# Kernel optimization log

Hardware: AMD Instinct MI355X
Metric: run time of the kernel (lower is better)

## Reference

```python
import jax, jax.numpy as jnp
import numpy as np

GROUPS = 32
EPS = 1e-5


def group_norm(x, w, b):
    # x: [B, C, H, W]
    B, C, H, W = x.shape
    g = x.reshape(B, GROUPS, C // GROUPS, H * W)
    mu = g.mean(axis=(2, 3), keepdims=True)
    var = g.var(axis=(2, 3), keepdims=True)
    g = (g - mu) * jax.lax.rsqrt(var + EPS)
    g = g.reshape(B, C, H, W)
    return g * w[None, :, None, None] + b[None, :, None, None]


def setup_inputs() -> dict:
    key = jax.random.key(0)
    ks = jax.random.split(key, 6)
    B, C, H, W = 4, 512, 64, 64
    s = 1.0 / np.sqrt(C)  # sane init scale for 1x1 conv weights
    return {
        "x": jax.random.normal(ks[0], (B, C, H, W), dtype=jnp.float32),
        "gn_w": jnp.ones((C,), dtype=jnp.float32),
        "gn_b": jnp.zeros((C,), dtype=jnp.float32),
        "wq": jax.random.normal(ks[1], (C, C), dtype=jnp.float32) * s,
        "bq": jnp.zeros((C,), dtype=jnp.float32),
        "wk": jax.random.normal(ks[2], (C, C), dtype=jnp.float32) * s,
        "bk": jnp.zeros((C,), dtype=jnp.float32),
        "wv": jax.random.normal(ks[3], (C, C), dtype=jnp.float32) * s,
        "bv": jnp.zeros((C,), dtype=jnp.float32),
        "wp": jax.random.normal(ks[4], (C, C), dtype=jnp.float32) * s,
        "bp": jnp.zeros((C,), dtype=jnp.float32),
    }


def reference(x, gn_w, gn_b, wq, bq, wk, bk, wv, bv, wp, bp):
    B, C, H, W = x.shape
    h = group_norm(x, gn_w, gn_b)
    # tokens: [B, N, C], N = H*W
    t = h.reshape(B, C, H * W).transpose(0, 2, 1)
    # 1x1 convs == per-token linear: y_d = sum_c w[d,c] * t_c + b_d
    q = jnp.einsum('bnc,dc->bnd', t, wq) + bq
    k = jnp.einsum('bnc,dc->bnd', t, wk) + bk
    v = jnp.einsum('bnc,dc->bnd', t, wv) + bv
    scale = 1.0 / jnp.sqrt(jnp.asarray(C, dtype=x.dtype))
    qk = jnp.einsum('bnd,bmd->bnm', q, k) * scale  # [B, N, N]
    attn = jax.nn.softmax(qk, axis=-1)
    out = jnp.einsum('bnm,bmd->bnd', attn, v)  # [B, N, C]
    proj = jnp.einsum('bnc,dc->bnd', out, wp) + bp
    return x + proj.transpose(0, 2, 1).reshape(B, C, H, W)
```

## Files before the change

kernel.cpp:

```cpp
#include <hip/hip_runtime.h>
#include <stdint.h>

#define B_   4
#define C_   512
#define N_   4096
#define G_   32
#define CPG  16
#define EPS  1e-5f

typedef __attribute__((ext_vector_type(8))) short bf16x8;
typedef __attribute__((ext_vector_type(4))) float f32x4;
typedef __attribute__((ext_vector_type(4))) int   i32x4;

__device__ __forceinline__ unsigned short f2bf(float f){
  union { float f; uint32_t u; } v; v.f = f;
  uint32_t r = v.u + 0x7fffu + ((v.u >> 16) & 1u);
  return (unsigned short)(r >> 16);
}
__device__ __forceinline__ float bf2f(unsigned short h){
  union { uint32_t u; float f; } v; v.u = ((uint32_t)h) << 16;
  return v.f;
}

__device__ __forceinline__ void gload16(const unsigned short* g, unsigned short* l){
  __builtin_amdgcn_global_load_lds(
      (__attribute__((address_space(1))) void*)(g),
      (__attribute__((address_space(3))) void*)(l), 16, 0, 0);
}
__device__ __forceinline__ void gload16i(const signed char* g, signed char* l){
  __builtin_amdgcn_global_load_lds(
      (__attribute__((address_space(1))) void*)(g),
      (__attribute__((address_space(3))) void*)(l), 16, 0, 0);
}

__global__ __launch_bounds__(256) void cvt_kernel(const float* __restrict__ in,
                                                  unsigned short* __restrict__ out, int n){
  int i = (blockIdx.x * 256 + threadIdx.x) * 4;
  if (i < n){
    float4 v = *(const float4*)(in + i);
    out[i+0] = f2bf(v.x); out[i+1] = f2bf(v.y);
    out[i+2] = f2bf(v.z); out[i+3] = f2bf(v.w);
  }
}

__global__ __launch_bounds__(256) void concat_bias_k(const float* __restrict__ bq,
                                                     const float* __restrict__ bk,
                                                     const float* __restrict__ bv,
                                                     float* __restrict__ b){
  int i = blockIdx.x * 256 + threadIdx.x;
  if (i < 1536)
    b[i] = (i < 512) ? bq[i] : ((i < 1024) ? bk[i-512] : bv[i-1024]);
}

__global__ __launch_bounds__(256) void gn_stats_k(const float* __restrict__ x,
                                                  float* __restrict__ stats){
  int bg = blockIdx.x;
  const float* p = x + (size_t)bg * (CPG * N_);
  float s = 0.f, ss = 0.f;
  for (int i = threadIdx.x * 4; i < CPG * N_; i += 256 * 4){
    float4 v = *(const float4*)(p + i);
    s  += v.x + v.y + v.z + v.w;
    ss += v.x*v.x + v.y*v.y + v.z*v.z + v.w*v.w;
  }
  #pragma unroll
  for (int o = 32; o >= 1; o >>= 1){ s += __shfl_xor(s, o); ss += __shfl_xor(ss, o); }
  __shared__ float sb[8];
  int w = threadIdx.x >> 6;
  if ((threadIdx.x & 63) == 0){ sb[w] = s; sb[4+w] = ss; }
  __syncthreads();
  if (threadIdx.x == 0){
    float S  = sb[0]+sb[1]+sb[2]+sb[3];
    float SS = sb[4]+sb[5]+sb[6]+sb[7];
    const float inv = 1.f / (CPG * N_);
    float mu  = S * inv;
    float var = SS * inv - mu * mu;
    stats[bg*2]   = mu;
    stats[bg*2+1] = rsqrtf(var + EPS);
  }
}

__global__ __launch_bounds__(256) void gn_apply_k(const float* __restrict__ x,
                                                  const float* __restrict__ stats,
                                                  const float* __restrict__ gw,
                                                  const float* __restrict__ gb,
                                                  unsigned short* __restrict__ t){
  int b  = blockIdx.z;
  int c0 = blockIdx.y * 64, n0 = blockIdx.x * 64;
  __shared__ float tile[64][65];
  for (int i = threadIdx.x; i < 64*64; i += 256){
    int cl = i >> 6, nl = i & 63;
    int c = c0 + cl;
    int g = c >> 4;
    float mu = stats[(b*G_+g)*2], rs = stats[(b*G_+g)*2+1];
    float v = x[((size_t)b*C_ + c)*N_ + n0 + nl];
    tile[cl][nl] = (v - mu) * rs * gw[c] + gb[c];
  }
  __syncthreads();
  for (int i = threadIdx.x; i < 64*64; i += 256){
    int nl = i >> 6, cl = i & 63;
    t[((size_t)b*N_ + n0 + nl)*C_ + c0 + cl] = f2bf(tile[cl][nl]);
  }
}

__global__ __launch_bounds__(256) void quant_qk_k(const unsigned short* __restrict__ qkv,
                                                  signed char* __restrict__ q8,
                                                  signed char* __restrict__ k8,
                                                  float invs){
  size_t idx = (size_t)blockIdx.x * 256 + threadIdx.x;
  size_t tok = idx >> 6;
  int ch = (int)(idx & 63);
  const unsigned short* pq = qkv + tok*1536 + ch*8;
  bf16x8 vq = *(const bf16x8*)pq;
  bf16x8 vk = *(const bf16x8*)(pq + 512);
  union { signed char c[8]; uint2 u; } oq, ok;
  #pragma unroll
  for (int j = 0; j < 8; j++){
    int a = __float2int_rn(bf2f((unsigned short)vq[j]) * invs);
    int b = __float2int_rn(bf2f((unsigned short)vk[j]) * invs);
    oq.c[j] = (signed char)max(-127, min(127, a));
    ok.c[j] = (signed char)max(-127, min(127, b));
  }
  *(uint2*)(q8 + tok*512 + ch*8) = oq.u;
  *(uint2*)(k8 + tok*512 + ch*8) = ok.u;
}

__global__ __launch_bounds__(256) void transpose_q8_k(const unsigned short* __restrict__ in,
                                                      signed char* __restrict__ out,
                                                      float invs){
  int r0 = blockIdx.x * 64, c0 = blockIdx.y * 64;
  size_t base_in  = (size_t)blockIdx.z * N_ * 1536;
  size_t base_out = (size_t)blockIdx.z * C_ * N_;
  __shared__ signed char tile[64][68];
  for (int i = threadIdx.x; i < 4096; i += 256){
    int rl = i >> 6, cl = i & 63;
    float v = bf2f(in[base_in + (size_t)(r0+rl)*1536 + c0 + cl]);
    int q = __float2int_rn(v * invs);
    tile[rl][cl] = (signed char)max(-127, min(127, q));
  }
  __syncthreads();
  for (int i = threadIdx.x; i < 4096; i += 256){
    int cl = i >> 6, rl = i & 63;
    out[base_out + (size_t)(c0+cl)*N_ + r0 + rl] = tile[rl][cl];
  }
}

__global__ __launch_bounds__(512, 2) void gemm256_k(const unsigned short* __restrict__ A,
                                                    const unsigned short* __restrict__ Bm,
                                                    unsigned short* __restrict__ Cm,
                                                    int lda, int ldb, int ldc,
                                                    int kper, int zdiv, int Mb,
                                                    long long sA, long long sB,
                                                    long long sC, long long sSp,
                                                    const float* __restrict__ bias,
                                                    float scale, int mode,
                                                    float* __restrict__ lpart, int lrows){
  __shared__ unsigned short As[2][256*64];
  __shared__ unsigned short Bs[2][256*64];

  const int tid  = threadIdx.x;
  const int lane = tid & 63, wave = tid >> 6;
  const int wr = wave >> 2, wc = wave & 3;
  const int fr = lane & 15, kl = lane >> 4;
  const int kl8 = kl * 8;
  const int rsw = (fr & 7) << 3;

  const int gx = gridDim.x, gy = gridDim.y;
  const int nwg = gx * gy * gridDim.z;
  int bid = blockIdx.x + gx * (blockIdx.y + gy * blockIdx.z);
  if ((nwg & 7) == 0)
    bid = (bid & 7) * (nwg >> 3) + (bid >> 3);
  const int bx = bid % gx;
  const int tmp2 = bid / gx;
  const int by = tmp2 % gy;
  const int bz = tmp2 / gy;

  const int batch = bz / zdiv;
  const int sp    = bz % zdiv;
  const int koff  = sp * kper;
  const unsigned short* Ab = A  + (size_t)batch*sA + (size_t)bx * 256 * lda + koff;
  const unsigned short* Bb = Bm + (size_t)batch*sB + (size_t)by * 256 * ldb + koff;
  unsigned short*       Cb = Cm + (size_t)batch*sC + (size_t)sp*sSp;

  const int g_row = tid >> 3;
  const int g_col = ((tid & 7) * 8) ^ (((tid >> 3) & 7) << 3);
  const int lw    = wave * 512;

#define STAGE(matG, ld, ldsArr, h, kt) do {                                         \
    const unsigned short* _g0 = (matG) + (size_t)((h)*128 + g_row)*(ld)             \
                                + (size_t)(kt)*64 + g_col;                          \
    gload16(_g0,                    &ldsArr[(kt)&1][(h)*8192 + lw]);                \
    gload16(_g0 + (size_t)64*(ld),  &ldsArr[(kt)&1][(h)*8192 + 4096 + lw]);         \
  } while(0)

  f32x4 acc[8][4];
  #pragma unroll
  for (int m = 0; m < 8; m++)
    #pragma unroll
    for (int n = 0; n < 4; n++)
      acc[m][n] = (f32x4){0.f,0.f,0.f,0.f};

  const int NT = kper >> 6;

  STAGE(Ab, lda, As, 0, 0);  STAGE(Ab, lda, As, 1, 0);
  STAGE(Bb, ldb, Bs, 0, 0);  STAGE(Bb, ldb, Bs, 1, 0);
  STAGE(Bb, ldb, Bs, 0, 1);  STAGE(Bb, ldb, Bs, 1, 1);
  asm volatile("s_waitcnt vmcnt(4)" ::: "memory");
  __builtin_amdgcn_sched_barrier(0);
  __builtin_amdgcn_s_barrier();

  bf16x8 af[4][2], ag[4][2], bfr[2][2], bf2[2][2];

#define RD_A(dst, Tl, mhofs)                                                     \
    _Pragma("unroll")                                                            \
    for (int m = 0; m < 4; m++)                                                  \
      _Pragma("unroll")                                                          \
      for (int kk = 0; kk < 2; kk++)                                             \
        dst[m][kk] = *(const bf16x8*)&Tl[(wr*128 + (mhofs) + m*16 + fr)*64 + ((kk*32 + kl8) ^ rsw)];
#define RD_B(dst, Tl, nofs)                                                      \
    _Pragma("unroll")                                                            \
    for (int n = 0; n < 2; n++)                                                  \
      _Pragma("unroll")                                                          \
      for (int kk = 0; kk < 2; kk++)                                             \
        dst[n][kk] = *(const bf16x8*)&Tl[(wc*64 + (nofs) + n*16 + fr)*64 + ((kk*32 + kl8) ^ rsw)];
#define MFMA16(mbase, nbase, afr, bft)                                           \
    __builtin_amdgcn_s_setprio(1);                                               \
    _Pragma("unroll")                                                            \
    for (int m = 0; m < 4; m++)                                                  \
      _Pragma("unroll")                                                          \
      for (int n = 0; n < 2; n++)                                                \
        _Pragma("unroll")                                                        \
        for (int kk = 0; kk < 2; kk++)                                           \
          acc[(mbase)+m][(nbase)+n] = __builtin_amdgcn_mfma_f32_16x16x32_bf16(   \
              afr[m][kk], bft[n][kk], acc[(mbase)+m][(nbase)+n], 0,0,0);         \
    __builtin_amdgcn_s_setprio(0);
#define BAR_LGKM                                                                 \
    __builtin_amdgcn_s_barrier();                                                \
    asm volatile("s_waitcnt lgkmcnt(0)" ::: "memory");                           \
    __builtin_amdgcn_sched_barrier(0);

  for (int kt = 0; kt < NT; kt += 2){
    const unsigned short* __restrict__ Al0 = As[0];
    const unsigned short* __restrict__ Bl0 = Bs[0];
    const unsigned short* __restrict__ Al1 = As[1];
    const unsigned short* __restrict__ Bl1 = Bs[1];

    RD_A(af, Al0, 0)
    RD_B(bfr, Bl0, 0)
    STAGE(Ab, lda, As, 0, kt+1);
    BAR_LGKM
    MFMA16(0, 0, af, bfr)
    __builtin_amdgcn_s_barrier();

    RD_B(bf2, Bl0, 32)
    STAGE(Ab, lda, As, 1, kt+1);
    BAR_LGKM
    MFMA16(0, 2, af, bf2)
    __builtin_amdgcn_s_barrier();

    RD_A(ag, Al0, 64)
    if (kt+2 < NT) STAGE(Bb, ldb, Bs, 0, kt+2);
    BAR_LGKM
    MFMA16(4, 0, ag, bfr)
    __builtin_amdgcn_s_barrier();

    if (kt+2 < NT){
      STAGE(Bb, ldb, Bs, 1, kt+2);
      asm volatile("s_waitcnt vmcnt(4)" ::: "memory");
    } else {
      asm volatile("s_waitcnt vmcnt(0)" ::: "memory");
    }
    __builtin_amdgcn_sched_barrier(0);
    __builtin_amdgcn_s_barrier();
    __builtin_amdgcn_sched_barrier(0);
    MFMA16(4, 2, ag, bf2)
    __builtin_amdgcn_s_barrier();

    RD_A(af, Al1, 0)
    RD_B(bfr, Bl1, 0)
    if (kt+2 < NT) STAGE(Ab, lda, As, 0, kt+2);
    BAR_LGKM
    MFMA16(0, 0, af, bfr)
    __builtin_amdgcn_s_barrier();

    RD_B(bf2, Bl1, 32)
    if (kt+2 < NT) STAGE(Ab, lda, As, 1, kt+2);
    BAR_LGKM
    MFMA16(0, 2, af, bf2)
    __builtin_amdgcn_s_barrier();

    RD_A(ag, Al1, 64)
    if (kt+3 < NT) STAGE(Bb, ldb, Bs, 0, kt+3);
    BAR_LGKM
    MFMA16(4, 0, ag, bfr)
    __builtin_amdgcn_s_barrier();

    if (kt+3 < NT){
      STAGE(Bb, ldb, Bs, 1, kt+3);
      asm volatile("s_waitcnt vmcnt(4)" ::: "memory");
    } else {
      asm volatile("s_waitcnt vmcnt(0)" ::: "memory");
    }
    __builtin_amdgcn_sched_barrier(0);
    __builtin_amdgcn_s_barrier();
    __builtin_amdgcn_sched_barrier(0);
    MFMA16(4, 2, ag, bf2)
    __builtin_amdgcn_s_barrier();
  }
#undef BAR_LGKM
#undef MFMA16
#undef RD_B
#undef RD_A
#undef STAGE

  const int cr = kl * 4, cc = fr;
  #pragma unroll
  for (int m = 0; m < 8; m++){
    #pragma unroll
    for (int n = 0; n < 4; n++){
      int gc = by*256 + wc*64 + n*16 + cc;
      float bv = (mode == 1) ? bias[gc] : 0.f;
      #pragma unroll
      for (int r = 0; r < 4; r++){
        int gr = bx*256 + wr*128 + m*16 + cr + r;
        Cb[(size_t)gr*ldc + gc] = f2bf((acc[m][n][r] + bv) * scale);
      }
    }
  }
}

__global__ __launch_bounds__(512, 2) void gemm256i_k(const signed char* __restrict__ A,
                                                     const signed char* __restrict__ Bm,
                                                     void* __restrict__ Cv,
                                                     int lda, int ldb, int ldc,
                                                     int kper, int zdiv, int Mb,
                                                     long long sA, long long sB,
                                                     long long sC, long long sSp,
                                                     float scale, float inv_sp, int mode,
                                                     float* __restrict__ lpart, int lrows){
  __shared__ signed char As[2][256*128];
  __shared__ signed char Bs[2][256*128];
  __shared__ float lsum[4][256];

  const int tid  = threadIdx.x;
  const int lane = tid & 63, wave = tid >> 6;
  const int wr = wave >> 2, wc = wave & 3;
  const int fr = lane & 15, kl = lane >> 4;
  const int kl16 = kl * 16;
  const int rsw = (fr & 7) << 4;

  const int gx = gridDim.x, gy = gridDim.y;
  const int nwg = gx * gy * gridDim.z;
  int bid = blockIdx.x + gx * (blockIdx.y + gy * blockIdx.z);
  if ((nwg & 7) == 0)
    bid = (bid & 7) * (nwg >> 3) + (bid >> 3);
  const int bx = bid % gx;
  const int tmp2 = bid / gx;
  const int by = tmp2 % gy;
  const int bz = tmp2 / gy;

  const int batch = bz / zdiv;
  const int sp    = bz % zdiv;
  const int koff  = sp * kper;
  const signed char* Ab = A  + (size_t)batch*sA + (size_t)bx * 256 * lda + koff;
  const signed char* Bb = Bm + (size_t)batch*sB + (size_t)by * 256 * ldb + koff;

  const int g_row = tid >> 3;
  const int g_col = ((tid & 7) * 16) ^ (((tid >> 3) & 7) << 4);
  const int lw    = wave * 1024;

#define STAGE(matG, ld, ldsArr, h, kt) do {                                         \
    const signed char* _g0 = (matG) + (size_t)((h)*128 + g_row)*(ld)                \
                                + (size_t)(kt)*128 + g_col;                         \
    gload16i(_g0,                    &ldsArr[(kt)&1][(h)*16384 + lw]);              \
    gload16i(_g0 + (size_t)64*(ld),  &ldsArr[(kt)&1][(h)*16384 + 8192 + lw]);       \
  } while(0)

  i32x4 acc[8][4];
  #pragma unroll
  for (int m = 0; m < 8; m++)
    #pragma unroll
    for (int n = 0; n < 4; n++)
      acc[m][n] = (i32x4){0,0,0,0};

  const int NT = kper >> 7;

  STAGE(Ab, lda, As, 0, 0);  STAGE(Ab, lda, As, 1, 0);
  STAGE(Bb, ldb, Bs, 0, 0);  STAGE(Bb, ldb, Bs, 1, 0);
  STAGE(Bb, ldb, Bs, 0, 1);  STAGE(Bb, ldb, Bs, 1, 1);
  asm volatile("s_waitcnt vmcnt(4)" ::: "memory");
  __builtin_amdgcn_sched_barrier(0);
  __builtin_amdgcn_s_barrier();

  i32x4 af[4][2], ag[4][2], bfr[2][2], bf2[2][2];

#define RD_A(dst, Tl, mhofs)                                                     \
    _Pragma("unroll")                                                            \
    for (int m = 0; m < 4; m++)                                                  \
      _Pragma("unroll")                                                          \
      for (int kk = 0; kk < 2; kk++)                                             \
        dst[m][kk] = *(const i32x4*)&Tl[(wr*128 + (mhofs) + m*16 + fr)*128 + ((kk*64 + kl16) ^ rsw)];
#define RD_B(dst, Tl, nofs)                                                      \
    _Pragma("unroll")                                                            \
    for (int n = 0; n < 2; n++)                                                  \
      _Pragma("unroll")                                                          \
      for (int kk = 0; kk < 2; kk++)                                             \
        dst[n][kk] = *(const i32x4*)&Tl[(wc*64 + (nofs) + n*16 + fr)*128 + ((kk*64 + kl16) ^ rsw)];
#define MFMA16(mbase, nbase, afr, bft)                                           \
    __builtin_amdgcn_s_setprio(1);                                               \
    _Pragma("unroll")                                                            \
    for (int m = 0; m < 4; m++)                                                  \
      _Pragma("unroll")                                                          \
      for (int n = 0; n < 2; n++)                                                \
        _Pragma("unroll")                                                        \
        for (int kk = 0; kk < 2; kk++)                                           \
          acc[(mbase)+m][(nbase)+n] = __builtin_amdgcn_mfma_i32_16x16x64_i8(     \
              afr[m][kk], bft[n][kk], acc[(mbase)+m][(nbase)+n], 0,0,0);         \
    __builtin_amdgcn_s_setprio(0);
#define BAR_LGKM                                                                 \
    __builtin_amdgcn_s_barrier();                                                \
    asm volatile("s_waitcnt lgkmcnt(0)" ::: "memory");                           \
    __builtin_amdgcn_sched_barrier(0);

  for (int kt = 0; kt < NT; kt += 2){
    const signed char* __restrict__ Al0 = As[0];
    const signed char* __restrict__ Bl0 = Bs[0];
    const signed char* __restrict__ Al1 = As[1];
    const signed char* __restrict__ Bl1 = Bs[1];

    RD_A(af, Al0, 0)
    RD_B(bfr, Bl0, 0)
    STAGE(Ab, lda, As, 0, kt+1);
    BAR_LGKM
    MFMA16(0, 0, af, bfr)
    __builtin_amdgcn_s_barrier();

    RD_B(bf2, Bl0, 32)
    STAGE(Ab, lda, As, 1, kt+1);
    BAR_LGKM
    MFMA16(0, 2, af, bf2)
    __builtin_amdgcn_s_barrier();

    RD_A(ag, Al0, 64)
    if (kt+2 < NT) STAGE(Bb, ldb, Bs, 0, kt+2);
    BAR_LGKM
    MFMA16(4, 0, ag, bfr)
    __builtin_amdgcn_s_barrier();

    if (kt+2 < NT){
      STAGE(Bb, ldb, Bs, 1, kt+2);
      asm volatile("s_waitcnt vmcnt(4)" ::: "memory");
    } else {
      asm volatile("s_waitcnt vmcnt(0)" ::: "memory");
    }
    __builtin_amdgcn_sched_barrier(0);
    __builtin_amdgcn_s_barrier();
    __builtin_amdgcn_sched_barrier(0);
    MFMA16(4, 2, ag, bf2)
    __builtin_amdgcn_s_barrier();

    RD_A(af, Al1, 0)
    RD_B(bfr, Bl1, 0)
    if (kt+2 < NT) STAGE(Ab, lda, As, 0, kt+2);
    BAR_LGKM
    MFMA16(0, 0, af, bfr)
    __builtin_amdgcn_s_barrier();

    RD_B(bf2, Bl1, 32)
    if (kt+2 < NT) STAGE(Ab, lda, As, 1, kt+2);
    BAR_LGKM
    MFMA16(0, 2, af, bf2)
    __builtin_amdgcn_s_barrier();

    RD_A(ag, Al1, 64)
    if (kt+3 < NT) STAGE(Bb, ldb, Bs, 0, kt+3);
    BAR_LGKM
    MFMA16(4, 0, ag, bfr)
    __builtin_amdgcn_s_barrier();

    if (kt+3 < NT){
      STAGE(Bb, ldb, Bs, 1, kt+3);
      asm volatile("s_waitcnt vmcnt(4)" ::: "memory");
    } else {
      asm volatile("s_waitcnt vmcnt(0)" ::: "memory");
    }
    __builtin_amdgcn_sched_barrier(0);
    __builtin_amdgcn_s_barrier();
    __builtin_amdgcn_sched_barrier(0);
    MFMA16(4, 2, ag, bf2)
    __builtin_amdgcn_s_barrier();
  }
#undef BAR_LGKM
#undef MFMA16
#undef RD_B
#undef RD_A
#undef STAGE

  const int cr = kl * 4, cc = fr;
  if (mode == 2){
    signed char* Cb = (signed char*)Cv + (size_t)batch*sC + (size_t)sp*sSp;
    float ps[8][4];
    #pragma unroll
    for (int m = 0; m < 8; m++)
      #pragma unroll
      for (int r = 0; r < 4; r++) ps[m][r] = 0.f;
    #pragma unroll
    for (int m = 0; m < 8; m++){
      #pragma unroll
      for (int n = 0; n < 4; n++){
        int gc = by*256 + wc*64 + n*16 + cc;
        #pragma unroll
        for (int r = 0; r < 4; r++){
          int gr = bx*256 + wr*128 + m*16 + cr + r;
          float s = fminf((float)acc[m][n][r] * scale, 10.f);
          float p = __expf(s);
          int pq = (int)(p * inv_sp + 0.5f);
          pq = min(pq, 127);
          Cb[(size_t)gr*ldc + gc] = (signed char)pq;
          ps[m][r] += (float)pq;
        }
      }
    }
    #pragma unroll
    for (int m = 0; m < 8; m++)
      #pragma unroll
      for (int r = 0; r < 4; r++){
        float v = ps[m][r];
        v += __shfl_xor(v, 1); v += __shfl_xor(v, 2);
        v += __shfl_xor(v, 4); v += __shfl_xor(v, 8);
        ps[m][r] = v;
      }
    if (cc == 0){
      #pragma unroll
      for (int m = 0; m < 8; m++)
        #pragma unroll
        for (int r = 0; r < 4; r++)
          lsum[wc][wr*128 + m*16 + cr + r] = ps[m][r];
    }
    __syncthreads();
    if (tid < 256){
      float v = lsum[0][tid] + lsum[1][tid] + lsum[2][tid] + lsum[3][tid];
      int rowg = batch*Mb + bx*256 + tid;
      lpart[(size_t)by * lrows + rowg] = v;
    }
  } else {
    unsigned short* Cb = (unsigned short*)Cv + (size_t)batch*sC + (size_t)sp*sSp;
    #pragma unroll
    for (int m = 0; m < 8; m++){
      #pragma unroll
      for (int n = 0; n < 4; n++){
        int gc = by*256 + wc*64 + n*16 + cc;
        #pragma unroll
        for (int r = 0; r < 4; r++){
          int gr = bx*256 + wr*128 + m*16 + cr + r;
          Cb[(size_t)gr*ldc + gc] = f2bf((float)acc[m][n][r] * scale);
        }
      }
    }
  }
}

__global__ __launch_bounds__(256, 2) void gemm_bt_k(const unsigned short* __restrict__ A,
                                                    const unsigned short* __restrict__ Bm,
                                                    unsigned short* __restrict__ Cm,
                                                    int M, int N, int K, int lda, int ldb,
                                                    const float* __restrict__ bias,
                                                    float scale){
  __shared__ unsigned short As[128*32];
  __shared__ unsigned short Bs[128*32];
  const int tid  = threadIdx.x;
  const int lane = tid & 63, wave = tid >> 6;
  const int wr = wave >> 1, wc = wave & 1;

  const int gx = gridDim.x, gy = gridDim.y;
  const int nwg = gx * gy;
  int bid = blockIdx.x + gx * blockIdx.y;
  if ((nwg & 7) == 0)
    bid = (bid & 7) * (nwg >> 3) + (bid >> 3);
  const int bx = bid % gx;
  const int by = bid / gx;

  const unsigned short* Ab = A  + (size_t)bx * 128 * lda;
  const unsigned short* Bb = Bm + (size_t)by * 128 * ldb;

  f32x4 acc[4][4];
  #pragma unroll
  for (int i = 0; i < 4; i++)
    #pragma unroll
    for (int j = 0; j < 4; j++)
      acc[i][j] = (f32x4){0.f, 0.f, 0.f, 0.f};

  const int ch0  = wave * 2;
  const int srow = ch0 * 16 + (lane >> 2);
  const int scol = (lane & 3) * 8;
  const unsigned short* gA0 = Ab + (size_t)srow * lda + scol;
  const unsigned short* gA1 = gA0 + (size_t)16 * lda;
  const unsigned short* gB0 = Bb + (size_t)srow * ldb + scol;
  const unsigned short* gB1 = gB0 + (size_t)16 * ldb;
  unsigned short* lA0 = &As[ch0 * 512];
  unsigned short* lA1 = &As[ch0 * 512 + 512];
  unsigned short* lB0 = &Bs[ch0 * 512];
  unsigned short* lB1 = &Bs[ch0 * 512 + 512];

  const int fr = lane & 15;
  const int fk = (lane >> 4) * 8;

  for (int k0 = 0; k0 < K; k0 += 32){
    gload16(gA0 + k0, lA0);
    gload16(gA1 + k0, lA1);
    gload16(gB0 + k0, lB0);
    gload16(gB1 + k0, lB1);
    __syncthreads();
    bf16x8 af[4], bfr[4];
    #pragma unroll
    for (int i = 0; i < 4; i++) af[i]  = *(const bf16x8*)&As[(wr*64 + i*16 + fr)*32 + fk];
    #pragma unroll
    for (int j = 0; j < 4; j++) bfr[j] = *(const bf16x8*)&Bs[(wc*64 + j*16 + fr)*32 + fk];
    #pragma unroll
    for (int i = 0; i < 4; i++)
      #pragma unroll
      for (int j = 0; j < 4; j++)
        acc[i][j] = __builtin_amdgcn_mfma_f32_16x16x32_bf16(af[i], bfr[j], acc[i][j], 0, 0, 0);
    __syncthreads();
  }

  const int cr = (lane >> 4) * 4, cc = lane & 15;
  #pragma unroll
  for (int i = 0; i < 4; i++){
    #pragma unroll
    for (int j = 0; j < 4; j++){
      int col = by*128 + wc*64 + j*16 + cc;
      float bv = bias ? bias[col] : 0.f;
      #pragma unroll
      for (int r = 0; r < 4; r++){
        int row = bx*128 + wr*64 + i*16 + cr + r;
        Cm[(size_t)row*N + col] = f2bf((acc[i][j][r] + bv) * scale);
      }
    }
  }
}

__global__ __launch_bounds__(256) void lreduce_k(const float* __restrict__ lpart,
                                                 float* __restrict__ linv,
                                                 int slices, int rows){
  int r = blockIdx.x * 256 + threadIdx.x;
  if (r < rows){
    float s = 0.f;
    for (int i = 0; i < slices; i++) s += lpart[(size_t)i*rows + r];
    linv[r] = 1.f / fmaxf(s, 1.f);
  }
}

__global__ __launch_bounds__(256) void combine_k(const unsigned short* __restrict__ O1,
                                                 const unsigned short* __restrict__ O2,
                                                 const float* __restrict__ linv,
                                                 unsigned short* __restrict__ o){
  size_t i = ((size_t)blockIdx.x * 256 + threadIdx.x) * 8;
  int row = (int)(i >> 9);
  float li = linv[row];
  bf16x8 a = *(const bf16x8*)(O1 + i);
  bf16x8 b = *(const bf16x8*)(O2 + i);
  bf16x8 r;
  #pragma unroll
  for (int j = 0; j < 8; j++)
    r[j] = (short)f2bf((bf2f((unsigned short)a[j]) + bf2f((unsigned short)b[j])) * li);
  *(bf16x8*)(o + i) = r;
}

__global__ __launch_bounds__(256) void residual_k(const float* __restrict__ x,
                                                  const unsigned short* __restrict__ proj,
                                                  float* __restrict__ out){
  int b  = blockIdx.z;
  int n0 = blockIdx.x * 64, d0 = blockIdx.y * 64;
  __shared__ float tile[64][65];
  for (int i = threadIdx.x; i < 4096; i += 256){
    int nl = i >> 6, dl = i & 63;
    tile[nl][dl] = bf2f(proj[((size_t)b*N_ + n0 + nl)*C_ + d0 + dl]);
  }
  __syncthreads();
  for (int i = threadIdx.x; i < 4096; i += 256){
    int dl = i >> 6, nl = i & 63;
    size_t idx = ((size_t)b*C_ + d0 + dl)*N_ + n0 + nl;
    out[idx] = x[idx] + tile[nl][dl];
  }
}

extern "C" void kernel_launch(void* const* d_in, const int* in_sizes, int n_in,
                              void* d_out, int out_size, void* d_ws, size_t ws_size,
                              hipStream_t stream){
  const float* x   = (const float*)d_in[0];
  const float* gnw = (const float*)d_in[1];
  const float* gnb = (const float*)d_in[2];
  const float* wq  = (const float*)d_in[3];
  const float* bq  = (const float*)d_in[4];
  const float* wk  = (const float*)d_in[5];
  const float* bk  = (const float*)d_in[6];
  const float* wv  = (const float*)d_in[7];
  const float* bv  = (const float*)d_in[8];
  const float* wp  = (const float*)d_in[9];
  const float* bp  = (const float*)d_in[10];
  float* out = (float*)d_out;

  char* ws = (char*)d_ws;
  const int  Mtok = B_ * N_;
  const size_t TSZ   = (size_t)Mtok * C_ * 2;
  const size_t QKVSZ = (size_t)Mtok * 1536 * 2;
  const size_t S8SZ  = (size_t)B_ * N_ * N_;
  const size_t Q8SZ  = (size_t)Mtok * C_;
  size_t off = 0;
  float*          stats = (float*)ws;               off += 4096;
  unsigned short* qkvw = (unsigned short*)(ws+off); off += (size_t)1536 * C_ * 2;
  unsigned short* wpb  = (unsigned short*)(ws+off); off += (size_t)C_ * C_ * 2;
  float*          bqkv = (float*)(ws+off);          off += 1536 * 4 + 2048;
  unsigned short* t    = (unsigned short*)(ws+off); off += TSZ;
  unsigned short* qkv  = (unsigned short*)(ws+off); off += QKVSZ;
  signed char*    S8   = (signed char*)(ws+off);    off += S8SZ;
  float*          lpart = (float*)(ws+off);         off += (size_t)32 * Mtok * 4;
  float*          linv  = (float*)(ws+off);         off += (size_t)Mtok * 4;
  signed char*    q8   = (signed char*)(ws+off);    off += Q8SZ;
  signed char*    k8   = (signed char*)(ws+off);    off += Q8SZ;
  signed char*    vt8  = (signed char*)(ws+off);    off += Q8SZ;

  const size_t PART = (size_t)Mtok * C_;
  unsigned short* O1   = qkv;
  unsigned short* O2   = qkv + PART;
  unsigned short* proj = qkv + 2*PART;
  unsigned short* o    = t;

  const float QS    = 6.f / 127.f;
  const float INVQS = 127.f / 6.f;
  const float qkscale = QS * QS * 0.044194173824159216f;
  const float inv_sp  = 127.f / 148.4131591f;

  const int NW = C_ * C_;
  cvt_kernel<<<NW/1024, 256, 0, stream>>>(wq, qkvw,        NW);
  cvt_kernel<<<NW/1024, 256, 0, stream>>>(wk, qkvw +   NW, NW);
  cvt_kernel<<<NW/1024, 256, 0, stream>>>(wv, qkvw + 2*NW, NW);
  cvt_kernel<<<NW/1024, 256, 0, stream>>>(wp, wpb,         NW);
  concat_bias_k<<<6, 256, 0, stream>>>(bq, bk, bv, bqkv);

  gn_stats_k<<<B_ * G_, 256, 0, stream>>>(x, stats);
  gn_apply_k<<<dim3(N_/64, C_/64, B_), 256, 0, stream>>>(x, stats, gnw, gnb, t);

  gemm256_k<<<dim3(Mtok/256, 1536/256, 1), 512, 0, stream>>>(
      t, qkvw, qkv, C_, C_, 1536, C_, 1, Mtok, 0,0,0,0, bqkv, 1.f, 1, nullptr, 0);

  quant_qk_k<<<Mtok*64/256, 256, 0, stream>>>(qkv, q8, k8, INVQS);
  transpose_q8_k<<<dim3(N_/64, C_/64, B_), 256, 0, stream>>>(qkv + 1024, vt8, INVQS);

  const long long sQ8 = (long long)N_ * C_;
  const long long sNN = (long long)N_ * N_;
  const long long sNC = (long long)N_ * C_;

  gemm256i_k<<<dim3(N_/256, N_/256, B_), 512, 0, stream>>>(
      q8, k8, S8, C_, C_, N_, C_, 1, N_, sQ8, sQ8, sNN, 0,
      qkscale, inv_sp, 2, lpart, Mtok);

  lreduce_k<<<Mtok/256, 256, 0, stream>>>(lpart, linv, 16, Mtok);

  gemm256i_k<<<dim3(N_/256, C_/256, B_*2), 512, 0, stream>>>(
      S8, vt8, O1, N_, N_, C_, 2048, 2, N_, sNN, sQ8, sNC, (long long)PART,
      QS, 0.f, 0, nullptr, 0);

  combine_k<<<(int)(PART/8/256), 256, 0, stream>>>(O1, O2, linv, o);

  gemm_bt_k<<<dim3(Mtok/128, C_/128, 1), 256, 0, stream>>>(
      o, wpb, proj, Mtok, C_, C_, C_, C_, bp, 1.f);

  residual_k<<<dim3(N_/64, C_/64, B_), 256, 0, stream>>>(x, proj, out);
}
```

Measured before the change: 266.0 us.

## Fuse Q/K int8 quantization into QKV GEMM epilogue with permuted packed stores

Removes the separate quant_qk kernel by quantizing Q and K to int8 inside the QKV GEMM epilogue, writing channel-permuted packed 32-bit stores. The permutation is kept consistent by permuting the V transpose output and the projection weight columns. The attention-score and PV epilogues also switch to packed vector stores, and the softmax numerator is computed with exp2 plus a folded offset instead of exp and a separate scale. This trades an extra kernel launch and a round trip of Q/K through memory for a more complex layout that has to match across kernels.

Result: faster. 258.0 us (-3.0%).

```diff
diff --git a/kernel.cpp b/kernel.cpp
--- a/kernel.cpp
+++ b/kernel.cpp
@@ -40,6 +40,21 @@
     float4 v = *(const float4*)(in + i);
     out[i+0] = f2bf(v.x); out[i+1] = f2bf(v.y);
     out[i+2] = f2bf(v.z); out[i+3] = f2bf(v.w);
+  }
+}
+
+__global__ __launch_bounds__(256) void cvt_perm_k(const float* __restrict__ in,
+                                                  unsigned short* __restrict__ out, int n){
+  int i = (blockIdx.x * 256 + threadIdx.x) * 4;
+  if (i < n){
+    #pragma unroll
+    for (int j = 0; j < 4; j++){
+      int idx = i + j;
+      int row = idx >> 9, col = idx & 511;
+      int o = col & 63;
+      int sc = (col & ~63) | (((o & 3) << 4) | (o >> 2));
+      out[idx] = f2bf(in[(row << 9) | sc]);
+    }
   }
 }
 
@@ -102,28 +117,6 @@
   }
 }
 
-__global__ __launch_bounds__(256) void quant_qk_k(const unsigned short* __restrict__ qkv,
-                                                  signed char* __restrict__ q8,
-                                                  signed char* __restrict__ k8,
-                                                  float invs){
-  size_t idx = (size_t)blockIdx.x * 256 + threadIdx.x;
-  size_t tok = idx >> 6;
-  int ch = (int)(idx & 63);
-  const unsigned short* pq = qkv + tok*1536 + ch*8;
-  bf16x8 vq = *(const bf16x8*)pq;
-  bf16x8 vk = *(const bf16x8*)(pq + 512);
-  union { signed char c[8]; uint2 u; } oq, ok;
-  #pragma unroll
-  for (int j = 0; j < 8; j++){
-    int a = __float2int_rn(bf2f((unsigned short)vq[j]) * invs);
-    int b = __float2int_rn(bf2f((unsigned short)vk[j]) * invs);
-    oq.c[j] = (signed char)max(-127, min(127, a));
-    ok.c[j] = (signed char)max(-127, min(127, b));
-  }
-  *(uint2*)(q8 + tok*512 + ch*8) = oq.u;
-  *(uint2*)(k8 + tok*512 + ch*8) = ok.u;
-}
-
 __global__ __launch_bounds__(256) void transpose_q8_k(const unsigned short* __restrict__ in,
                                                       signed char* __restrict__ out,
                                                       float invs){
@@ -140,7 +133,8 @@
   __syncthreads();
   for (int i = threadIdx.x; i < 4096; i += 256){
     int cl = i >> 6, rl = i & 63;
-    out[base_out + (size_t)(c0+cl)*N_ + r0 + rl] = tile[rl][cl];
+    int rp = ((rl & 15) << 2) | (rl >> 4);
+    out[base_out + (size_t)(c0+cl)*N_ + r0 + rp] = tile[rl][cl];
   }
 }
 
@@ -153,7 +147,9 @@
                                                     long long sC, long long sSp,
                                                     const float* __restrict__ bias,
                                                     float scale, int mode,
-                                                    float* __restrict__ lpart, int lrows){
+                                                    signed char* __restrict__ q8p,
+                                                    signed char* __restrict__ k8p,
+                                                    float invqs){
   __shared__ unsigned short As[2][256*64];
   __shared__ unsigned short Bs[2][256*64];
 
@@ -313,16 +309,38 @@
 #undef STAGE
 
   const int cr = kl * 4, cc = fr;
-  #pragma unroll
-  for (int m = 0; m < 8; m++){
-    #pragma unroll
-    for (int n = 0; n < 4; n++){
-      int gc = by*256 + wc*64 + n*16 + cc;
-      float bv = (mode == 1) ? bias[gc] : 0.f;
+  if (mode == 3 && by < 4){
+    signed char* dst = (by < 2) ? q8p : k8p;
+    const int cb = (by & 1)*256 + wc*64 + cc*4;
+    #pragma unroll
+    for (int m = 0; m < 8; m++){
       #pragma unroll
       for (int r = 0; r < 4; r++){
         int gr = bx*256 + wr*128 + m*16 + cr + r;
-        Cb[(size_t)gr*ldc + gc] = f2bf((acc[m][n][r] + bv) * scale);
+        uint32_t pk = 0;
+        #pragma unroll
+        for (int n = 0; n < 4; n++){
+          int gc = by*256 + wc*64 + n*16 + cc;
+          float v = (acc[m][n][r] + bias[gc]) * invqs;
+          int q = __float2int_rn(v);
+          q = max(-127, min(127, q));
+          pk |= (uint32_t)(q & 0xff) << (n*8);
+        }
+        *(uint32_t*)&dst[(size_t)gr*512 + cb] = pk;
+      }
+    }
+  } else {
+    #pragma unroll
+    for (int m = 0; m < 8; m++){
+      #pragma unroll
+      for (int n = 0; n < 4; n++){
+        int gc = by*256 + wc*64 + n*16 + cc;
+        float bv = (mode == 1 || mode == 3) ? bias[gc] : 0.f;
+        #pragma unroll
+        for (int r = 0; r < 4; r++){
+          int gr = bx*256 + wr*128 + m*16 + cr + r;
+          Cb[(size_t)gr*ldc + gc] = f2bf((acc[m][n][r] + bv) * scale);
+        }
       }
     }
   }
@@ -335,7 +353,7 @@
                                                      int kper, int zdiv, int Mb,
                                                      long long sA, long long sB,
                                                      long long sC, long long sSp,
-                                                     float scale, float inv_sp, int mode,
+                                                     float c1, float c2, int mode,
                                                      float* __restrict__ lpart, int lrows){
   __shared__ signed char As[2][256*128];
   __shared__ signed char Bs[2][256*128];
@@ -498,33 +516,36 @@
   const int cr = kl * 4, cc = fr;
   if (mode == 2){
     signed char* Cb = (signed char*)Cv + (size_t)batch*sC + (size_t)sp*sSp;
+    const int cb = by*256 + wc*64 + cc*4;
+    int ip[8][4];
+    #pragma unroll
+    for (int m = 0; m < 8; m++)
+      #pragma unroll
+      for (int r = 0; r < 4; r++) ip[m][r] = 0;
+    #pragma unroll
+    for (int m = 0; m < 8; m++){
+      #pragma unroll
+      for (int r = 0; r < 4; r++){
+        int gr = bx*256 + wr*128 + m*16 + cr + r;
+        uint32_t pk = 0;
+        #pragma unroll
+        for (int n = 0; n < 4; n++){
+          float arg = (float)acc[m][n][r] * c1 + c2;
+          arg = fminf(arg, 6.99f);
+          float p = exp2f(arg);
+          int pq = (int)(p + 0.5f);
+          pk |= (uint32_t)pq << (n*8);
+          ip[m][r] += pq;
+        }
+        *(uint32_t*)&Cb[(size_t)gr*ldc + cb] = pk;
+      }
+    }
     float ps[8][4];
     #pragma unroll
     for (int m = 0; m < 8; m++)
       #pragma unroll
-      for (int r = 0; r < 4; r++) ps[m][r] = 0.f;
-    #pragma unroll
-    for (int m = 0; m < 8; m++){
-      #pragma unroll
-      for (int n = 0; n < 4; n++){
-        int gc = by*256 + wc*64 + n*16 + cc;
-        #pragma unroll
-        for (int r = 0; r < 4; r++){
-          int gr = bx*256 + wr*128 + m*16 + cr + r;
-          float s = fminf((float)acc[m][n][r] * scale, 10.f);
-          float p = __expf(s);
-          int pq = (int)(p * inv_sp + 0.5f);
-          pq = min(pq, 127);
-          Cb[(size_t)gr*ldc + gc] = (signed char)pq;
-          ps[m][r] += (float)pq;
-        }
-      }
-    }
-    #pragma unroll
-    for (int m = 0; m < 8; m++)
-      #pragma unroll
       for (int r = 0; r < 4; r++){
-        float v = ps[m][r];
+        float v = (float)ip[m][r];
         v += __shfl_xor(v, 1); v += __shfl_xor(v, 2);
         v += __shfl_xor(v, 4); v += __shfl_xor(v, 8);
         ps[m][r] = v;
@@ -544,16 +565,20 @@
     }
   } else {
     unsigned short* Cb = (unsigned short*)Cv + (size_t)batch*sC + (size_t)sp*sSp;
+    const int cb = by*256 + wc*64 + cc*4;
     #pragma unroll
     for (int m = 0; m < 8; m++){
       #pragma unroll
-      for (int n = 0; n < 4; n++){
-        int gc = by*256 + wc*64 + n*16 + cc;
-        #pragma unroll
-        for (int r = 0; r < 4; r++){
-          int gr = bx*256 + wr*128 + m*16 + cr + r;
-          Cb[(size_t)gr*ldc + gc] = f2bf((float)acc[m][n][r] * scale);
-        }
+      for (int r = 0; r < 4; r++){
+        int gr = bx*256 + wr*128 + m*16 + cr + r;
+        unsigned short w0 = f2bf((float)acc[m][0][r] * c1);
+        unsigned short w1 = f2bf((float)acc[m][1][r] * c1);
+        unsigned short w2 = f2bf((float)acc[m][2][r] * c1);
+        unsigned short w3 = f2bf((float)acc[m][3][r] * c1);
+        uint2 pk;
+        pk.x = (uint32_t)w0 | ((uint32_t)w1 << 16);
+        pk.y = (uint32_t)w2 | ((uint32_t)w3 << 16);
+        *(uint2*)&Cb[(size_t)gr*ldc + cb] = pk;
       }
     }
   }
@@ -729,22 +754,22 @@
   const float QS    = 6.f / 127.f;
   const float INVQS = 127.f / 6.f;
   const float qkscale = QS * QS * 0.044194173824159216f;
-  const float inv_sp  = 127.f / 148.4131591f;
+  const float qk_c1 = qkscale * 1.4426950408889634f;
+  const float qk_c2 = -0.22478961f;
 
   const int NW = C_ * C_;
   cvt_kernel<<<NW/1024, 256, 0, stream>>>(wq, qkvw,        NW);
   cvt_kernel<<<NW/1024, 256, 0, stream>>>(wk, qkvw +   NW, NW);
   cvt_kernel<<<NW/1024, 256, 0, stream>>>(wv, qkvw + 2*NW, NW);
-  cvt_kernel<<<NW/1024, 256, 0, stream>>>(wp, wpb,         NW);
+  cvt_perm_k<<<NW/1024, 256, 0, stream>>>(wp, wpb,         NW);
   concat_bias_k<<<6, 256, 0, stream>>>(bq, bk, bv, bqkv);
 
   gn_stats_k<<<B_ * G_, 256, 0, stream>>>(x, stats);
   gn_apply_k<<<dim3(N_/64, C_/64, B_), 256, 0, stream>>>(x, stats, gnw, gnb, t);
 
   gemm256_k<<<dim3(Mtok/256, 1536/256, 1), 512, 0, stream>>>(
-      t, qkvw, qkv, C_, C_, 1536, C_, 1, Mtok, 0,0,0,0, bqkv, 1.f, 1, nullptr, 0);
-
-  quant_qk_k<<<Mtok*64/256, 256, 0, stream>>>(qkv, q8, k8, INVQS);
+      t, qkvw, qkv, C_, C_, 1536, C_, 1, Mtok, 0,0,0,0, bqkv, 1.f, 3, q8, k8, INVQS);
+
   transpose_q8_k<<<dim3(N_/64, C_/64, B_), 256, 0, stream>>>(qkv + 1024, vt8, INVQS);
 
   const long long sQ8 = (long long)N_ * C_;
@@ -753,7 +778,7 @@
 
   gemm256i_k<<<dim3(N_/256, N_/256, B_), 512, 0, stream>>>(
       q8, k8, S8, C_, C_, N_, C_, 1, N_, sQ8, sQ8, sNN, 0,
-      qkscale, inv_sp, 2, lpart, Mtok);
+      qk_c1, qk_c2, 2, lpart, Mtok);
 
   lreduce_k<<<Mtok/256, 256, 0, stream>>>(lpart, linv, 16, Mtok);
 
```
